# Kernel tuning notes

Hardware: AMD Instinct MI355X
Metric: run time of the kernel (lower is better)

Reference implementation:

```python
import jax, jax.numpy as jnp
import numpy as np

G = 256          # voxel grid extent per axis
N = 2_000_000    # number of occupied (unique) voxels
K = 3            # kernel size per axis -> 27 offsets


def setup_inputs() -> dict:
    # Unique sparse voxel coordinates in a G^3 grid (MinkowskiEngine requires unique coords).
    rng = np.random.default_rng(0)
    lin = rng.choice(G ** 3, size=N, replace=False).astype(np.int64)
    x = (lin // (G * G)).astype(np.int32)
    y = ((lin // G) % G).astype(np.int32)
    z = (lin % G).astype(np.int32)
    coords = jnp.stack([jnp.asarray(x), jnp.asarray(y), jnp.asarray(z)], axis=1)  # (N,3) int32

    key = jax.random.key(0)
    k1, k2 = jax.random.split(key)
    feats = jax.random.normal(k1, (N, 1), dtype=jnp.float32)          # (N, C_in=1)
    W = jax.random.normal(k2, (K ** 3, 1, 1), dtype=jnp.float32) * 0.2  # (27, C_in, C_out), ME layout; bias=False default
    return {"coords": coords, "feats": feats, "W": W}


def _encode(c):
    # linearize 3D integer coords -> unique int64 key
    return (c[..., 0].astype(jnp.int64) * G + c[..., 1]) * G + c[..., 2]


def reference(coords, feats, W):
    # Sparse 3x3x3 convolution, stride 1: out[i] = sum_k W[k] @ feats[neighbor(i, offset_k)]
    # Neighbor lookup = hash-map in ME; here: sorted-key binary search (gather-GEMM-scatter).
    n = coords.shape[0]
    keys = _encode(coords)                       # (N,)
    order = jnp.argsort(keys)
    skeys = keys[order]                          # sorted keys

    r = jnp.arange(-1, 2)
    off = jnp.stack(jnp.meshgrid(r, r, r, indexing="ij"), axis=-1).reshape(27, 3)  # (27,3)

    nc = coords[None, :, :] + off[:, None, :]    # (27, N, 3) neighbor coords
    valid = jnp.all((nc >= 0) & (nc < G), axis=-1)  # (27, N)
    nk = _encode(nc)                             # (27, N)

    pos = jnp.searchsorted(skeys, nk.reshape(-1)).reshape(27, n)
    pos = jnp.clip(pos, 0, n - 1)
    found = valid & (skeys[pos] == nk)           # neighbor exists in sparse set
    j = order[pos]                               # (27, N) gather indices into feats

    gathered = jnp.where(found[..., None], feats[j], 0.0)  # (27, N, C_in)
    out = jnp.einsum("kni,kio->no", gathered, W)           # (N, C_out)
    return out
```

## Files before the change

kernel.cpp:

```cpp
#include <hip/hip_runtime.h>
#include <hip/hip_bf16.h>


#define GEXT 256
#define GRID_CELLS (1u << 24)
#define GRID_BYTES ((size_t)GRID_CELLS * 2)

typedef __attribute__((ext_vector_type(8))) unsigned short ushort8v;

__device__ __forceinline__ float bf16_to_f32(unsigned short b) {
    return __uint_as_float(((unsigned)b) << 16);
}
__device__ __forceinline__ unsigned short f32_to_bf16(float f) {
    unsigned u = __float_as_uint(f);
    u += 0x7fffu + ((u >> 16) & 1u);
    return (unsigned short)(u >> 16);
}

__global__ void scatter_k(const int* __restrict__ coords,
                          const float* __restrict__ feats,
                          unsigned short* __restrict__ grid, int n) {
    int i = blockIdx.x * blockDim.x + threadIdx.x;
    if (i >= n) return;
    unsigned x = (unsigned)coords[3 * i + 0];
    unsigned y = (unsigned)coords[3 * i + 1];
    unsigned z = (unsigned)coords[3 * i + 2];
    grid[(x << 16) | (y << 8) | z] = f32_to_bf16(feats[i]);
}

__global__ __launch_bounds__(256) void conv_k(const unsigned short* __restrict__ gin,
                                              const float* __restrict__ W,
                                              unsigned short* __restrict__ gout) {
    __shared__ float sW[27];
    if (threadIdx.x < 27) sW[threadIdx.x] = W[threadIdx.x];
    __syncthreads();

    int bid = blockIdx.x;
    int x  = bid >> 5;
    int y  = (bid & 31) * 8 + (threadIdx.x >> 5);
    int z0 = (threadIdx.x & 31) * 8;

    float acc[8];
#pragma unroll
    for (int j = 0; j < 8; ++j) acc[j] = 0.0f;

#pragma unroll
    for (int dx = -1; dx <= 1; ++dx) {
        int xx = x + dx;
        if ((unsigned)xx >= (unsigned)GEXT) continue;
#pragma unroll
        for (int dy = -1; dy <= 1; ++dy) {
            int yy = y + dy;
            if ((unsigned)yy >= (unsigned)GEXT) continue;
            const unsigned short* row = gin + (((unsigned)xx << 16) | ((unsigned)yy << 8));

            ushort8v mid = *(const ushort8v*)(row + z0);
            float v[10];
            v[0] = (z0 > 0)   ? bf16_to_f32(row[z0 - 1]) : 0.0f;
#pragma unroll
            for (int j = 0; j < 8; ++j) v[j + 1] = bf16_to_f32(mid[j]);
            v[9] = (z0 < 248) ? bf16_to_f32(row[z0 + 8]) : 0.0f;

            int kb = ((dx + 1) * 3 + (dy + 1)) * 3;
            float w0 = sW[kb + 0], w1 = sW[kb + 1], w2 = sW[kb + 2];
#pragma unroll
            for (int j = 0; j < 8; ++j)
                acc[j] += w0 * v[j] + w1 * v[j + 1] + w2 * v[j + 2];
        }
    }

    ushort8v o;
#pragma unroll
    for (int j = 0; j < 8; ++j) o[j] = f32_to_bf16(acc[j]);
    *(ushort8v*)(gout + (((unsigned)x << 16) | ((unsigned)y << 8) | (unsigned)z0)) = o;
}

__global__ void gather_out_k(const int* __restrict__ coords,
                             const unsigned short* __restrict__ gout,
                             float* __restrict__ out, int n) {
    int i = blockIdx.x * blockDim.x + threadIdx.x;
    if (i >= n) return;
    unsigned x = (unsigned)coords[3 * i + 0];
    unsigned y = (unsigned)coords[3 * i + 1];
    unsigned z = (unsigned)coords[3 * i + 2];
    out[i] = bf16_to_f32(gout[(x << 16) | (y << 8) | z]);
}

extern "C" void kernel_launch(void* const* d_in, const int* in_sizes, int n_in,
                              void* d_out, int out_size, void* d_ws, size_t ws_size,
                              hipStream_t stream) {
    const int*   coords = (const int*)d_in[0];
    const float* feats  = (const float*)d_in[1];
    const float* W      = (const float*)d_in[2];
    float*       out    = (float*)d_out;

    int n = in_sizes[1];
    unsigned short* gin  = (unsigned short*)d_ws;
    unsigned short* gout = (unsigned short*)((char*)d_ws + GRID_BYTES);

    (void)hipMemsetAsync(gin, 0, GRID_BYTES, stream);

    const int bs = 256;
    int nb = (n + bs - 1) / bs;
    scatter_k<<<nb, bs, 0, stream>>>(coords, feats, gin, n);
    conv_k<<<8192, 256, 0, stream>>>(gin, W, gout);
    gather_out_k<<<nb, bs, 0, stream>>>(coords, gout, out, n);
}
```

Before: 189.8 us.

## Fuse output gather into conv via index grid and use lane shuffles for halos

Scatter now also writes a per-cell index grid, so the conv kernel can write fp32 outputs straight to their sparse positions. This drops the bf16 output grid and the separate gather kernel. Z-halo values are exchanged with warp shuffles instead of extra scalar loads, and weights are read directly from global memory. In exchange, the index grid adds a 64MB memset and a 64MB read, and the path depends on there being enough workspace.

Measured after the change: 179.2 us. 1.06x faster.

```diff
diff --git a/kernel.cpp b/kernel.cpp
--- a/kernel.cpp
+++ b/kernel.cpp
@@ -4,9 +4,11 @@
 
 #define GEXT 256
 #define GRID_CELLS (1u << 24)
-#define GRID_BYTES ((size_t)GRID_CELLS * 2)
+#define GIN_BYTES ((size_t)GRID_CELLS * 2)
+#define IDX_BYTES ((size_t)GRID_CELLS * 4)
 
 typedef __attribute__((ext_vector_type(8))) unsigned short ushort8v;
+typedef __attribute__((ext_vector_type(4))) int int4v;
 
 __device__ __forceinline__ float bf16_to_f32(unsigned short b) {
     return __uint_as_float(((unsigned)b) << 16);
@@ -17,33 +19,37 @@
     return (unsigned short)(u >> 16);
 }
 
-__global__ void scatter_k(const int* __restrict__ coords,
-                          const float* __restrict__ feats,
-                          unsigned short* __restrict__ grid, int n) {
+__global__ void scatter_fused_k(const int* __restrict__ coords,
+                                const float* __restrict__ feats,
+                                unsigned short* __restrict__ gin,
+                                int* __restrict__ idx, int n) {
     int i = blockIdx.x * blockDim.x + threadIdx.x;
     if (i >= n) return;
     unsigned x = (unsigned)coords[3 * i + 0];
     unsigned y = (unsigned)coords[3 * i + 1];
     unsigned z = (unsigned)coords[3 * i + 2];
-    grid[(x << 16) | (y << 8) | z] = f32_to_bf16(feats[i]);
+    unsigned cell = (x << 16) | (y << 8) | z;
+    gin[cell] = f32_to_bf16(feats[i]);
+    idx[cell] = i + 1;
 }
 
-__global__ __launch_bounds__(256) void conv_k(const unsigned short* __restrict__ gin,
-                                              const float* __restrict__ W,
-                                              unsigned short* __restrict__ gout) {
-    __shared__ float sW[27];
-    if (threadIdx.x < 27) sW[threadIdx.x] = W[threadIdx.x];
-    __syncthreads();
+__global__ void scatter_k(const int* __restrict__ coords,
+                          const float* __restrict__ feats,
+                          unsigned short* __restrict__ gin, int n) {
+    int i = blockIdx.x * blockDim.x + threadIdx.x;
+    if (i >= n) return;
+    unsigned x = (unsigned)coords[3 * i + 0];
+    unsigned y = (unsigned)coords[3 * i + 1];
+    unsigned z = (unsigned)coords[3 * i + 2];
+    gin[(x << 16) | (y << 8) | z] = f32_to_bf16(feats[i]);
+}
 
-    int bid = blockIdx.x;
-    int x  = bid >> 5;
-    int y  = (bid & 31) * 8 + (threadIdx.x >> 5);
-    int z0 = (threadIdx.x & 31) * 8;
-
-    float acc[8];
+__device__ __forceinline__ void stencil8(const unsigned short* __restrict__ gin,
+                                         const float* __restrict__ W,
+                                         int x, int y, int z0, int lane,
+                                         float acc[8]) {
 #pragma unroll
     for (int j = 0; j < 8; ++j) acc[j] = 0.0f;
-
 #pragma unroll
     for (int dx = -1; dx <= 1; ++dx) {
         int xx = x + dx;
@@ -52,22 +58,61 @@
         for (int dy = -1; dy <= 1; ++dy) {
             int yy = y + dy;
             if ((unsigned)yy >= (unsigned)GEXT) continue;
-            const unsigned short* row = gin + (((unsigned)xx << 16) | ((unsigned)yy << 8));
-
+            const unsigned short* row =
+                gin + (((unsigned)xx << 16) | ((unsigned)yy << 8));
             ushort8v mid = *(const ushort8v*)(row + z0);
             float v[10];
-            v[0] = (z0 > 0)   ? bf16_to_f32(row[z0 - 1]) : 0.0f;
 #pragma unroll
             for (int j = 0; j < 8; ++j) v[j + 1] = bf16_to_f32(mid[j]);
-            v[9] = (z0 < 248) ? bf16_to_f32(row[z0 + 8]) : 0.0f;
-
-            int kb = ((dx + 1) * 3 + (dy + 1)) * 3;
-            float w0 = sW[kb + 0], w1 = sW[kb + 1], w2 = sW[kb + 2];
+            float up = __shfl_up(v[8], 1, 32);
+            float dn = __shfl_down(v[1], 1, 32);
+            v[0] = (lane == 0)  ? 0.0f : up;
+            v[9] = (lane == 31) ? 0.0f : dn;
+            int kb = (dx + 1) * 9 + (dy + 1) * 3;
+            float w0 = W[kb], w1 = W[kb + 1], w2 = W[kb + 2];
 #pragma unroll
             for (int j = 0; j < 8; ++j)
                 acc[j] += w0 * v[j] + w1 * v[j + 1] + w2 * v[j + 2];
         }
     }
+}
+
+__global__ __launch_bounds__(256) void conv_out_k(const unsigned short* __restrict__ gin,
+                                                  const int* __restrict__ idx,
+                                                  const float* __restrict__ W,
+                                                  float* __restrict__ out) {
+    int bid = blockIdx.x;
+    int x  = bid >> 5;
+    int y  = (bid & 31) * 8 + (threadIdx.x >> 5);
+    int z0 = (threadIdx.x & 31) * 8;
+    int lane = threadIdx.x & 31;
+
+    unsigned c0 = ((unsigned)x << 16) | ((unsigned)y << 8) | (unsigned)z0;
+    int4v i0 = *(const int4v*)(idx + c0);
+    int4v i1 = *(const int4v*)(idx + c0 + 4);
+
+    float acc[8];
+    stencil8(gin, W, x, y, z0, lane, acc);
+
+#pragma unroll
+    for (int j = 0; j < 4; ++j)
+        if (i0[j]) out[i0[j] - 1] = acc[j];
+#pragma unroll
+    for (int j = 0; j < 4; ++j)
+        if (i1[j]) out[i1[j] - 1] = acc[j + 4];
+}
+
+__global__ __launch_bounds__(256) void conv_gout_k(const unsigned short* __restrict__ gin,
+                                                   const float* __restrict__ W,
+                                                   unsigned short* __restrict__ gout) {
+    int bid = blockIdx.x;
+    int x  = bid >> 5;
+    int y  = (bid & 31) * 8 + (threadIdx.x >> 5);
+    int z0 = (threadIdx.x & 31) * 8;
+    int lane = threadIdx.x & 31;
+
+    float acc[8];
+    stencil8(gin, W, x, y, z0, lane, acc);
 
     ushort8v o;
 #pragma unroll
@@ -95,14 +140,21 @@
     float*       out    = (float*)d_out;
 
     int n = in_sizes[1];
-    unsigned short* gin  = (unsigned short*)d_ws;
-    unsigned short* gout = (unsigned short*)((char*)d_ws + GRID_BYTES);
-
-    (void)hipMemsetAsync(gin, 0, GRID_BYTES, stream);
+    unsigned short* gin = (unsigned short*)d_ws;
 
     const int bs = 256;
     int nb = (n + bs - 1) / bs;
-    scatter_k<<<nb, bs, 0, stream>>>(coords, feats, gin, n);
-    conv_k<<<8192, 256, 0, stream>>>(gin, W, gout);
-    gather_out_k<<<nb, bs, 0, stream>>>(coords, gout, out, n);
+
+    if (ws_size >= GIN_BYTES + IDX_BYTES) {
+        int* idx = (int*)((char*)d_ws + GIN_BYTES);
+        (void)hipMemsetAsync(d_ws, 0, GIN_BYTES + IDX_BYTES, stream);
+        scatter_fused_k<<<nb, bs, 0, stream>>>(coords, feats, gin, idx, n);
+        conv_out_k<<<8192, 256, 0, stream>>>(gin, idx, W, out);
+    } else {
+        unsigned short* gout = (unsigned short*)((char*)d_ws + GIN_BYTES);
+        (void)hipMemsetAsync(gin, 0, GIN_BYTES, stream);
+        scatter_k<<<nb, bs, 0, stream>>>(coords, feats, gin, n);
+        conv_gout_k<<<8192, 256, 0, stream>>>(gin, W, gout);
+        gather_out_k<<<nb, bs, 0, stream>>>(coords, gout, out, n);
+    }
 }
```
